# Performance work log

Measured on AMD Instinct MI355X. Metric: run time of the kernel, lower is better.

Reference implementation:

```python
import jax, jax.numpy as jnp
import numpy as np

B, LQ, LK, D = 16, 2048, 2048, 64
TEMPERATURE = 8.0  # sqrt(d_k)


def setup_inputs() -> dict:
    key = jax.random.key(0)
    kq, kk, kv, km = jax.random.split(key, 4)
    q = jax.random.normal(kq, (B, LQ, D), dtype=jnp.float32)
    k = jax.random.normal(kk, (B, LK, D), dtype=jnp.float32)
    v = jax.random.normal(kv, (B, LK, D), dtype=jnp.float32)
    mask = jax.random.randint(km, (B, LQ, LK), 0, 2).astype(jnp.bool_)
    return {"q": q, "k": k, "v": v, "mask": mask}


def reference(q, k, v, mask):
    # attn = bmm(q, k^T) / temperature  -> [B, LQ, LK]
    attn = jnp.einsum("bqd,bkd->bqk", q, k) / TEMPERATURE
    attn = jnp.where(mask, -jnp.inf, attn)
    attn = jax.nn.softmax(attn, axis=2)
    out = jnp.einsum("bqk,bkd->bqd", attn, v)  # [B, LQ, D]
    return out, attn
```

## Files before the change

kernel.cpp:

```cpp
#include <hip/hip_runtime.h>
#include <hip/hip_bf16.h>

namespace {
constexpr int kB = 16;
constexpr int kLQ = 2048;
constexpr int kLK = 2048;
constexpr int kD = 64;
constexpr int kQBlk = 16;
constexpr int kStride = 2056;
constexpr float kLog2e = 1.44269504088896340736f;
}

using short8 = __attribute__((ext_vector_type(8))) short;
using f32x4 = __attribute__((ext_vector_type(4))) float;

union S8U { short8 v; unsigned u[4]; unsigned long long q[2]; };

static __device__ __forceinline__ unsigned pk2(float lo, float hi) {
    __hip_bfloat162 h = __float22bfloat162_rn(float2{lo, hi});
    unsigned short a = __builtin_bit_cast(unsigned short, h.x);
    unsigned short b = __builtin_bit_cast(unsigned short, h.y);
    return (unsigned)a | ((unsigned)b << 16);
}
static __device__ __forceinline__ float bf2f(unsigned short s) {
    unsigned u = ((unsigned)s) << 16;
    return __builtin_bit_cast(float, u);
}
static __device__ __forceinline__ short8 cvt8(float4 a, float4 b) {
    S8U r;
    r.u[0] = pk2(a.x, a.y); r.u[1] = pk2(a.z, a.w);
    r.u[2] = pk2(b.x, b.y); r.u[3] = pk2(b.z, b.w);
    return r.v;
}

__global__ __launch_bounds__(512, 4) void sdpa_v5_kernel(
    const float* __restrict__ qg, const float* __restrict__ kg,
    const float* __restrict__ vg, const void* __restrict__ maskg,
    float* __restrict__ outg, float* __restrict__ attng)
{
    __shared__ unsigned short s_s[kQBlk][kStride];
    __shared__ float s_wsum[8][16];
    __shared__ float s_red[kQBlk][kD];
    __shared__ int s_flag;

    const int tid = threadIdx.x;
    const int wave = tid >> 6;
    const int lane = tid & 63;
    const int r16 = lane & 15;
    const int g = lane >> 4;

    const int blk = blockIdx.x;
    const int b = blk >> 7;
    const int qrow0 = (blk & 127) * kQBlk;

    if (tid < 64) {
        unsigned w = ((const unsigned*)maskg)[tid];
        unsigned long long bal = __ballot((w & 0xFFFFFF00u) != 0u);
        if (tid == 0) s_flag = (bal != 0ull) ? 1 : 0;
    }
    __syncthreads();
    const bool mask_byte = (s_flag != 0);
    const unsigned char* mask_u8 = (const unsigned char*)maskg;
    const int* mask_i32 = (const int*)maskg;

    short8 q0, q1;
    {
        const float4* qp = (const float4*)(qg + ((size_t)b * kLQ + qrow0 + r16) * kD);
        const float s = 0.125f * kLog2e;
        float4 x0 = qp[2*g + 0], x1 = qp[2*g + 1];
        float4 x2 = qp[2*g + 8], x3 = qp[2*g + 9];
        x0 *= s; x1 *= s; x2 *= s; x3 *= s;
        q0 = cvt8(x0, x1);
        q1 = cvt8(x2, x3);
    }
    const size_t kbase = (size_t)b * kLK * kD;
    const size_t mrowL = ((size_t)b * kLQ + qrow0 + r16) * (size_t)kLK;
    float wsum = 0.f;

    unsigned hmA[8], hmB[8];
    if (mask_byte) {
#pragma unroll
        for (int i = 0; i < 8; ++i) {
            const int c0 = (wave + 8 * i) * 32;
            hmA[i] = *(const unsigned*)(mask_u8 + mrowL + c0 + 4*g);
            hmB[i] = *(const unsigned*)(mask_u8 + mrowL + c0 + 16 + 4*g);
        }
    }

    float4 cur[8], nxt[8];
    {
        const int col0 = wave * 32;
        const float4* kpA = (const float4*)(kg + kbase + (size_t)(col0 + r16) * kD);
        const float4* kpB = (const float4*)(kg + kbase + (size_t)(col0 + 16 + r16) * kD);
        cur[0] = kpA[2*g]; cur[1] = kpA[2*g+1]; cur[2] = kpA[2*g+8]; cur[3] = kpA[2*g+9];
        cur[4] = kpB[2*g]; cur[5] = kpB[2*g+1]; cur[6] = kpB[2*g+8]; cur[7] = kpB[2*g+9];
    }
#pragma unroll
    for (int i = 0; i < 8; ++i) {
        const int t = wave + 8 * i;
        const int col0 = t * 32;
        if (i < 7) {
            const int nc0 = (t + 8) * 32;
            const float4* kpA = (const float4*)(kg + kbase + (size_t)(nc0 + r16) * kD);
            const float4* kpB = (const float4*)(kg + kbase + (size_t)(nc0 + 16 + r16) * kD);
            nxt[0] = kpA[2*g]; nxt[1] = kpA[2*g+1]; nxt[2] = kpA[2*g+8]; nxt[3] = kpA[2*g+9];
            nxt[4] = kpB[2*g]; nxt[5] = kpB[2*g+1]; nxt[6] = kpB[2*g+8]; nxt[7] = kpB[2*g+9];
        }
        const short8 kA0 = cvt8(cur[0], cur[1]);
        const short8 kA1 = cvt8(cur[2], cur[3]);
        const short8 kB0 = cvt8(cur[4], cur[5]);
        const short8 kB1 = cvt8(cur[6], cur[7]);
        f32x4 accA = {0.f, 0.f, 0.f, 0.f}, accB = {0.f, 0.f, 0.f, 0.f};
        accA = __builtin_amdgcn_mfma_f32_16x16x32_bf16(kA0, q0, accA, 0, 0, 0);
        accA = __builtin_amdgcn_mfma_f32_16x16x32_bf16(kA1, q1, accA, 0, 0, 0);
        accB = __builtin_amdgcn_mfma_f32_16x16x32_bf16(kB0, q0, accB, 0, 0, 0);
        accB = __builtin_amdgcn_mfma_f32_16x16x32_bf16(kB1, q1, accB, 0, 0, 0);

        const int cA = col0 + 4*g;
        const int cB = col0 + 16 + 4*g;
        unsigned mwA, mwB;
        if (mask_byte) {
            mwA = hmA[i]; mwB = hmB[i];
        } else {
            const int4 a = *(const int4*)(mask_i32 + mrowL + cA);
            const int4 c = *(const int4*)(mask_i32 + mrowL + cB);
            mwA = (a.x ? 1u : 0u) | (a.y ? 0x100u : 0u) | (a.z ? 0x10000u : 0u) | (a.w ? 0x1000000u : 0u);
            mwB = (c.x ? 1u : 0u) | (c.y ? 0x100u : 0u) | (c.z ? 0x10000u : 0u) | (c.w ? 0x1000000u : 0u);
        }
        float eA[4], eB[4];
#pragma unroll
        for (int r = 0; r < 4; ++r) {
            eA[r] = ((mwA >> (8*r)) & 0xFFu) ? 0.f : __builtin_amdgcn_exp2f(accA[r]);
            eB[r] = ((mwB >> (8*r)) & 0xFFu) ? 0.f : __builtin_amdgcn_exp2f(accB[r]);
        }
        wsum += (eA[0] + eA[1]) + (eA[2] + eA[3]) + (eB[0] + eB[1]) + (eB[2] + eB[3]);
        S8U pA, pB;
        pA.u[0] = pk2(eA[0], eA[1]); pA.u[1] = pk2(eA[2], eA[3]);
        pB.u[0] = pk2(eB[0], eB[1]); pB.u[1] = pk2(eB[2], eB[3]);
        *(unsigned long long*)&s_s[r16][cA] = pA.q[0];
        *(unsigned long long*)&s_s[r16][cB] = pB.q[0];
#pragma unroll
        for (int j = 0; j < 8; ++j) cur[j] = nxt[j];
    }
    wsum += __shfl_xor(wsum, 16, 64);
    wsum += __shfl_xor(wsum, 32, 64);
    if (g == 0) s_wsum[wave][r16] = wsum;
    __syncthreads();

    {
        const int rr = tid >> 5;
        const int cc = tid & 31;
        float rsum = 0.f;
#pragma unroll
        for (int w = 0; w < 8; ++w) rsum += s_wsum[w][rr];
        const float rinv = __builtin_amdgcn_rcpf(rsum);
        float* arow = attng + ((size_t)b * kLQ + qrow0 + rr) * kLK;
#pragma unroll 4
        for (int i = 0; i < 16; ++i) {
            const int col = cc * 4 + i * 128;
            const unsigned long long sv = *(const unsigned long long*)&s_s[rr][col];
            float4 a;
            a.x = bf2f((unsigned short)(sv >>  0)) * rinv;
            a.y = bf2f((unsigned short)(sv >> 16)) * rinv;
            a.z = bf2f((unsigned short)(sv >> 32)) * rinv;
            a.w = bf2f((unsigned short)(sv >> 48)) * rinv;
            *(float4*)(arow + col) = a;
        }
    }

    {
        const int d0 = (wave & 3) * 16;
        const int kh = wave >> 2;
        const float* vbase = vg + (size_t)b * kLK * kD + d0 + r16;
        float va[8], vb[8];
#pragma unroll
        for (int j = 0; j < 8; ++j) va[j] = vbase[(size_t)(kh*1024 + 8*g + j) * kD];
        f32x4 acc = {0.f, 0.f, 0.f, 0.f};
#pragma unroll
        for (int kt = 0; kt < 32; ++kt) {
            const int kk0 = (kh * 32 + kt) * 32 + 8 * g;
            float* cv = (kt & 1) ? vb : va;
            float* nv = (kt & 1) ? va : vb;
            if (kt < 31) {
#pragma unroll
                for (int j = 0; j < 8; ++j) nv[j] = vbase[(size_t)(kk0 + 32 + j) * kD];
            }
            const short8 af = *(const short8*)&s_s[r16][kk0];
            S8U bv;
            bv.u[0] = pk2(cv[0], cv[1]); bv.u[1] = pk2(cv[2], cv[3]);
            bv.u[2] = pk2(cv[4], cv[5]); bv.u[3] = pk2(cv[6], cv[7]);
            acc = __builtin_amdgcn_mfma_f32_16x16x32_bf16(af, bv.v, acc, 0, 0, 0);
        }
        if (kh == 1) {
#pragma unroll
            for (int r = 0; r < 4; ++r) s_red[4*g + r][d0 + r16] = acc[r];
        }
        __syncthreads();
        if (kh == 0) {
#pragma unroll
            for (int r = 0; r < 4; ++r) {
                const int m = 4*g + r;
                float rs = 0.f;
#pragma unroll
                for (int w = 0; w < 8; ++w) rs += s_wsum[w][m];
                outg[((size_t)b * kLQ + qrow0 + m) * kD + d0 + r16] =
                    (acc[r] + s_red[m][d0 + r16]) * __builtin_amdgcn_rcpf(rs);
            }
        }
    }
}

extern "C" void kernel_launch(void* const* d_in, const int* in_sizes, int n_in,
                              void* d_out, int out_size, void* d_ws, size_t ws_size,
                              hipStream_t stream) {
    (void)in_sizes; (void)n_in; (void)out_size; (void)d_ws; (void)ws_size;
    const float* q = (const float*)d_in[0];
    const float* k = (const float*)d_in[1];
    const float* v = (const float*)d_in[2];
    const void* mask = d_in[3];
    float* out = (float*)d_out;
    float* attn = out + (size_t)kB * kLQ * kD;
    const dim3 grid(kB * (kLQ / kQBlk));
    sdpa_v5_kernel<<<grid, 512, 0, stream>>>(q, k, v, mask, out, attn);
}
```

Measured before the change: 278.1 us.

## Split fused attention into QK-exp kernel and normalize-PV kernel

Replaces the single fused kernel with two kernels. The first tiles 64 query rows by 512 keys, stages K and mask in shared memory, writes unnormalized exp scores to the attn buffer and partial row sums into the out buffer. The second reads those back, normalizes them in place, and computes P·V. This adds a full extra read and write of the large attn matrix and a second launch, in exchange for K reuse across more query rows and lower shared-memory use per block.

```diff
diff --git a/kernel.cpp b/kernel.cpp
--- a/kernel.cpp
+++ b/kernel.cpp
@@ -6,15 +6,20 @@
 constexpr int kLQ = 2048;
 constexpr int kLK = 2048;
 constexpr int kD = 64;
-constexpr int kQBlk = 16;
-constexpr int kStride = 2056;
 constexpr float kLog2e = 1.44269504088896340736f;
+constexpr int kQT = 64;
+constexpr int kKT = 512;
+constexpr int kKStrB = 144;
+constexpr int kMStrB = 40;
+constexpr int kBStrB = 144;
+constexpr int kChunk = 256;
+constexpr int kEStrB = 528;
 }
 
 using short8 = __attribute__((ext_vector_type(8))) short;
 using f32x4 = __attribute__((ext_vector_type(4))) float;
 
-union S8U { short8 v; unsigned u[4]; unsigned long long q[2]; };
+union S8U { short8 v; unsigned u[4]; };
 
 static __device__ __forceinline__ unsigned pk2(float lo, float hi) {
     __hip_bfloat162 h = __float22bfloat162_rn(float2{lo, hi});
@@ -22,25 +27,15 @@
     unsigned short b = __builtin_bit_cast(unsigned short, h.y);
     return (unsigned)a | ((unsigned)b << 16);
 }
-static __device__ __forceinline__ float bf2f(unsigned short s) {
-    unsigned u = ((unsigned)s) << 16;
-    return __builtin_bit_cast(float, u);
-}
-static __device__ __forceinline__ short8 cvt8(float4 a, float4 b) {
-    S8U r;
-    r.u[0] = pk2(a.x, a.y); r.u[1] = pk2(a.z, a.w);
-    r.u[2] = pk2(b.x, b.y); r.u[3] = pk2(b.z, b.w);
-    return r.v;
-}
-
-__global__ __launch_bounds__(512, 4) void sdpa_v5_kernel(
+
+__global__ __launch_bounds__(256, 4) void k1_qke(
     const float* __restrict__ qg, const float* __restrict__ kg,
-    const float* __restrict__ vg, const void* __restrict__ maskg,
-    float* __restrict__ outg, float* __restrict__ attng)
+    const void* __restrict__ maskg, float* __restrict__ attng,
+    float* __restrict__ outg)
 {
-    __shared__ unsigned short s_s[kQBlk][kStride];
-    __shared__ float s_wsum[8][16];
-    __shared__ float s_red[kQBlk][kD];
+    __shared__ __align__(16) unsigned char s_kst[32 * kKStrB];
+    __shared__ __align__(16) unsigned char s_mst[64 * kMStrB];
+    __shared__ __align__(16) unsigned char s_bnc[4][16 * kBStrB];
     __shared__ int s_flag;
 
     const int tid = threadIdx.x;
@@ -51,7 +46,10 @@
 
     const int blk = blockIdx.x;
     const int b = blk >> 7;
-    const int qrow0 = (blk & 127) * kQBlk;
+    const int kt = (blk >> 5) & 3;
+    const int qt = blk & 31;
+    const int rows0 = qt * kQT;
+    const int c0 = kt * kKT;
 
     if (tid < 64) {
         unsigned w = ((const unsigned*)maskg)[tid];
@@ -65,147 +63,168 @@
 
     short8 q0, q1;
     {
-        const float4* qp = (const float4*)(qg + ((size_t)b * kLQ + qrow0 + r16) * kD);
+        const float4* qp = (const float4*)(qg + ((size_t)b * kLQ + rows0 + wave * 16 + r16) * kD);
         const float s = 0.125f * kLog2e;
         float4 x0 = qp[2*g + 0], x1 = qp[2*g + 1];
         float4 x2 = qp[2*g + 8], x3 = qp[2*g + 9];
         x0 *= s; x1 *= s; x2 *= s; x3 *= s;
-        q0 = cvt8(x0, x1);
-        q1 = cvt8(x2, x3);
-    }
-    const size_t kbase = (size_t)b * kLK * kD;
-    const size_t mrowL = ((size_t)b * kLQ + qrow0 + r16) * (size_t)kLK;
+        S8U a, c;
+        a.u[0] = pk2(x0.x, x0.y); a.u[1] = pk2(x0.z, x0.w);
+        a.u[2] = pk2(x1.x, x1.y); a.u[3] = pk2(x1.z, x1.w);
+        c.u[0] = pk2(x2.x, x2.y); c.u[1] = pk2(x2.z, x2.w);
+        c.u[2] = pk2(x3.x, x3.y); c.u[3] = pk2(x3.z, x3.w);
+        q0 = a.v; q1 = c.v;
+    }
+
     float wsum = 0.f;
 
-    unsigned hmA[8], hmB[8];
-    if (mask_byte) {
-#pragma unroll
-        for (int i = 0; i < 8; ++i) {
-            const int c0 = (wave + 8 * i) * 32;
-            hmA[i] = *(const unsigned*)(mask_u8 + mrowL + c0 + 4*g);
-            hmB[i] = *(const unsigned*)(mask_u8 + mrowL + c0 + 16 + 4*g);
-        }
-    }
-
-    float4 cur[8], nxt[8];
-    {
-        const int col0 = wave * 32;
-        const float4* kpA = (const float4*)(kg + kbase + (size_t)(col0 + r16) * kD);
-        const float4* kpB = (const float4*)(kg + kbase + (size_t)(col0 + 16 + r16) * kD);
-        cur[0] = kpA[2*g]; cur[1] = kpA[2*g+1]; cur[2] = kpA[2*g+8]; cur[3] = kpA[2*g+9];
-        cur[4] = kpB[2*g]; cur[5] = kpB[2*g+1]; cur[6] = kpB[2*g+8]; cur[7] = kpB[2*g+9];
-    }
-#pragma unroll
-    for (int i = 0; i < 8; ++i) {
-        const int t = wave + 8 * i;
-        const int col0 = t * 32;
-        if (i < 7) {
-            const int nc0 = (t + 8) * 32;
-            const float4* kpA = (const float4*)(kg + kbase + (size_t)(nc0 + r16) * kD);
-            const float4* kpB = (const float4*)(kg + kbase + (size_t)(nc0 + 16 + r16) * kD);
-            nxt[0] = kpA[2*g]; nxt[1] = kpA[2*g+1]; nxt[2] = kpA[2*g+8]; nxt[3] = kpA[2*g+9];
-            nxt[4] = kpB[2*g]; nxt[5] = kpB[2*g+1]; nxt[6] = kpB[2*g+8]; nxt[7] = kpB[2*g+9];
-        }
-        const short8 kA0 = cvt8(cur[0], cur[1]);
-        const short8 kA1 = cvt8(cur[2], cur[3]);
-        const short8 kB0 = cvt8(cur[4], cur[5]);
-        const short8 kB1 = cvt8(cur[6], cur[7]);
+    for (int sub = 0; sub < kKT / 32; ++sub) {
+        const int csub = c0 + sub * 32;
+        {
+            const int krow = tid >> 3;
+            const int d8 = (tid & 7) * 8;
+            const float4* kp = (const float4*)(kg + ((size_t)b * kLK + csub + krow) * kD + d8);
+            float4 y0 = kp[0], y1 = kp[1];
+            S8U p;
+            p.u[0] = pk2(y0.x, y0.y); p.u[1] = pk2(y0.z, y0.w);
+            p.u[2] = pk2(y1.x, y1.y); p.u[3] = pk2(y1.z, y1.w);
+            *(short8*)(s_kst + krow * kKStrB + d8 * 2) = p.v;
+        }
+        {
+            const int mrow = tid >> 2;
+            const int mc = (tid & 3) * 8;
+            unsigned long long f;
+            if (mask_byte) {
+                f = *(const unsigned long long*)(mask_u8 +
+                        ((size_t)b * kLQ + rows0 + mrow) * (size_t)kLK + csub + mc);
+            } else {
+                const int* mp = mask_i32 + ((size_t)b * kLQ + rows0 + mrow) * (size_t)kLK + csub + mc;
+                const int4 m0 = *(const int4*)mp;
+                const int4 m1 = *(const int4*)(mp + 4);
+                f  = (m0.x ? 1ull : 0ull)       | (m0.y ? 1ull << 8 : 0ull)
+                   | (m0.z ? 1ull << 16 : 0ull) | (m0.w ? 1ull << 24 : 0ull)
+                   | (m1.x ? 1ull << 32 : 0ull) | (m1.y ? 1ull << 40 : 0ull)
+                   | (m1.z ? 1ull << 48 : 0ull) | (m1.w ? 1ull << 56 : 0ull);
+            }
+            *(unsigned long long*)(s_mst + mrow * kMStrB + mc) = f;
+        }
+        __syncthreads();
+
+        const short8 kA0 = *(const short8*)(s_kst + r16 * kKStrB + g * 16);
+        const short8 kA1 = *(const short8*)(s_kst + r16 * kKStrB + 64 + g * 16);
+        const short8 kB0 = *(const short8*)(s_kst + (16 + r16) * kKStrB + g * 16);
+        const short8 kB1 = *(const short8*)(s_kst + (16 + r16) * kKStrB + 64 + g * 16);
         f32x4 accA = {0.f, 0.f, 0.f, 0.f}, accB = {0.f, 0.f, 0.f, 0.f};
         accA = __builtin_amdgcn_mfma_f32_16x16x32_bf16(kA0, q0, accA, 0, 0, 0);
         accA = __builtin_amdgcn_mfma_f32_16x16x32_bf16(kA1, q1, accA, 0, 0, 0);
         accB = __builtin_amdgcn_mfma_f32_16x16x32_bf16(kB0, q0, accB, 0, 0, 0);
         accB = __builtin_amdgcn_mfma_f32_16x16x32_bf16(kB1, q1, accB, 0, 0, 0);
 
-        const int cA = col0 + 4*g;
-        const int cB = col0 + 16 + 4*g;
-        unsigned mwA, mwB;
-        if (mask_byte) {
-            mwA = hmA[i]; mwB = hmB[i];
-        } else {
-            const int4 a = *(const int4*)(mask_i32 + mrowL + cA);
-            const int4 c = *(const int4*)(mask_i32 + mrowL + cB);
-            mwA = (a.x ? 1u : 0u) | (a.y ? 0x100u : 0u) | (a.z ? 0x10000u : 0u) | (a.w ? 0x1000000u : 0u);
-            mwB = (c.x ? 1u : 0u) | (c.y ? 0x100u : 0u) | (c.z ? 0x10000u : 0u) | (c.w ? 0x1000000u : 0u);
-        }
-        float eA[4], eB[4];
+        const unsigned mwA = *(const unsigned*)(s_mst + (wave * 16 + r16) * kMStrB + 4 * g);
+        const unsigned mwB = *(const unsigned*)(s_mst + (wave * 16 + r16) * kMStrB + 16 + 4 * g);
+        f32x4 eA, eB;
 #pragma unroll
         for (int r = 0; r < 4; ++r) {
             eA[r] = ((mwA >> (8*r)) & 0xFFu) ? 0.f : __builtin_amdgcn_exp2f(accA[r]);
             eB[r] = ((mwB >> (8*r)) & 0xFFu) ? 0.f : __builtin_amdgcn_exp2f(accB[r]);
         }
         wsum += (eA[0] + eA[1]) + (eA[2] + eA[3]) + (eB[0] + eB[1]) + (eB[2] + eB[3]);
-        S8U pA, pB;
-        pA.u[0] = pk2(eA[0], eA[1]); pA.u[1] = pk2(eA[2], eA[3]);
-        pB.u[0] = pk2(eB[0], eB[1]); pB.u[1] = pk2(eB[2], eB[3]);
-        *(unsigned long long*)&s_s[r16][cA] = pA.q[0];
-        *(unsigned long long*)&s_s[r16][cB] = pB.q[0];
-#pragma unroll
-        for (int j = 0; j < 8; ++j) cur[j] = nxt[j];
+        *(f32x4*)(s_bnc[wave] + r16 * kBStrB + g * 16) = eA;
+        *(f32x4*)(s_bnc[wave] + r16 * kBStrB + 64 + g * 16) = eB;
+        __syncthreads();
+
+        {
+            const int row = tid >> 2;
+            const int cseg = tid & 3;
+            const unsigned char* src = s_bnc[row >> 4] + (row & 15) * kBStrB + cseg * 32;
+            const f32x4 v0 = *(const f32x4*)src;
+            const f32x4 v1 = *(const f32x4*)(src + 16);
+            float* dst = attng + ((size_t)b * kLQ + rows0 + row) * (size_t)kLK + csub + cseg * 8;
+            *(f32x4*)dst = v0;
+            *(f32x4*)(dst + 4) = v1;
+        }
     }
     wsum += __shfl_xor(wsum, 16, 64);
     wsum += __shfl_xor(wsum, 32, 64);
-    if (g == 0) s_wsum[wave][r16] = wsum;
+    if (g == 0)
+        outg[((size_t)b * kLQ + rows0 + wave * 16 + r16) * kD + kt] = wsum;
+}
+
+__global__ __launch_bounds__(512, 2) void k2_norm_pv(
+    const float* __restrict__ vg, float* __restrict__ attng,
+    float* __restrict__ outg)
+{
+    __shared__ __align__(16) unsigned char s_e[16 * kEStrB];
+    __shared__ float s_red[16][kD];
+    __shared__ float s_rinv[16];
+
+    const int tid = threadIdx.x;
+    const int wave = tid >> 6;
+    const int lane = tid & 63;
+    const int r16 = lane & 15;
+    const int g = lane >> 4;
+
+    const int blk = blockIdx.x;
+    const int b = blk >> 7;
+    const int row0 = (blk & 127) * 16;
+
+    if (tid < 64) {
+        const int r = tid >> 2, p = tid & 3;
+        float ps = outg[((size_t)b * kLQ + row0 + r) * kD + p];
+        ps += __shfl_xor(ps, 1, 64);
+        ps += __shfl_xor(ps, 2, 64);
+        if (p == 0) s_rinv[r] = __builtin_amdgcn_rcpf(ps);
+    }
     __syncthreads();
 
-    {
-        const int rr = tid >> 5;
-        const int cc = tid & 31;
-        float rsum = 0.f;
-#pragma unroll
-        for (int w = 0; w < 8; ++w) rsum += s_wsum[w][rr];
-        const float rinv = __builtin_amdgcn_rcpf(rsum);
-        float* arow = attng + ((size_t)b * kLQ + qrow0 + rr) * kLK;
-#pragma unroll 4
-        for (int i = 0; i < 16; ++i) {
-            const int col = cc * 4 + i * 128;
-            const unsigned long long sv = *(const unsigned long long*)&s_s[rr][col];
-            float4 a;
-            a.x = bf2f((unsigned short)(sv >>  0)) * rinv;
-            a.y = bf2f((unsigned short)(sv >> 16)) * rinv;
-            a.z = bf2f((unsigned short)(sv >> 32)) * rinv;
-            a.w = bf2f((unsigned short)(sv >> 48)) * rinv;
-            *(float4*)(arow + col) = a;
-        }
-    }
-
-    {
-        const int d0 = (wave & 3) * 16;
-        const int kh = wave >> 2;
-        const float* vbase = vg + (size_t)b * kLK * kD + d0 + r16;
-        float va[8], vb[8];
-#pragma unroll
-        for (int j = 0; j < 8; ++j) va[j] = vbase[(size_t)(kh*1024 + 8*g + j) * kD];
-        f32x4 acc = {0.f, 0.f, 0.f, 0.f};
-#pragma unroll
-        for (int kt = 0; kt < 32; ++kt) {
-            const int kk0 = (kh * 32 + kt) * 32 + 8 * g;
-            float* cv = (kt & 1) ? vb : va;
-            float* nv = (kt & 1) ? va : vb;
-            if (kt < 31) {
-#pragma unroll
-                for (int j = 0; j < 8; ++j) nv[j] = vbase[(size_t)(kk0 + 32 + j) * kD];
-            }
-            const short8 af = *(const short8*)&s_s[r16][kk0];
+    const int d0 = (wave & 3) * 16;
+    const int kh = wave >> 2;
+    f32x4 acc = {0.f, 0.f, 0.f, 0.f};
+    const float* vbase = vg + (size_t)b * kLK * kD + d0 + r16;
+
+    for (int chunk = 0; chunk < kLK / kChunk; ++chunk) {
+        const int c0 = chunk * kChunk;
+        {
+            const int row = tid >> 5;
+            const int cc = tid & 31;
+            const float rinv = s_rinv[row];
+            float* ap = attng + ((size_t)b * kLQ + row0 + row) * (size_t)kLK + c0 + cc * 8;
+            f32x4 e0 = *(const f32x4*)ap;
+            f32x4 e1 = *(const f32x4*)(ap + 4);
+            e0 *= rinv; e1 *= rinv;
+            *(f32x4*)ap = e0;
+            *(f32x4*)(ap + 4) = e1;
+            S8U p;
+            p.u[0] = pk2(e0[0], e0[1]); p.u[1] = pk2(e0[2], e0[3]);
+            p.u[2] = pk2(e1[0], e1[1]); p.u[3] = pk2(e1[2], e1[3]);
+            *(short8*)(s_e + row * kEStrB + cc * 16) = p.v;
+        }
+        __syncthreads();
+#pragma unroll
+        for (int s = 0; s < 4; ++s) {
+            const int kk = kh * 128 + s * 32 + 8 * g;
+            const short8 af = *(const short8*)(s_e + r16 * kEStrB + kk * 2);
+            const float* vp = vbase + (size_t)(c0 + kk) * kD;
+            float v0 = vp[0*kD], v1 = vp[1*kD], v2 = vp[2*kD], v3 = vp[3*kD];
+            float v4 = vp[4*kD], v5 = vp[5*kD], v6 = vp[6*kD], v7 = vp[7*kD];
             S8U bv;
-            bv.u[0] = pk2(cv[0], cv[1]); bv.u[1] = pk2(cv[2], cv[3]);
-            bv.u[2] = pk2(cv[4], cv[5]); bv.u[3] = pk2(cv[6], cv[7]);
+            bv.u[0] = pk2(v0, v1); bv.u[1] = pk2(v2, v3);
+            bv.u[2] = pk2(v4, v5); bv.u[3] = pk2(v6, v7);
             acc = __builtin_amdgcn_mfma_f32_16x16x32_bf16(af, bv.v, acc, 0, 0, 0);
         }
-        if (kh == 1) {
-#pragma unroll
-            for (int r = 0; r < 4; ++r) s_red[4*g + r][d0 + r16] = acc[r];
-        }
-        __syncthreads();
-        if (kh == 0) {
-#pragma unroll
-            for (int r = 0; r < 4; ++r) {
-                const int m = 4*g + r;
-                float rs = 0.f;
-#pragma unroll
-                for (int w = 0; w < 8; ++w) rs += s_wsum[w][m];
-                outg[((size_t)b * kLQ + qrow0 + m) * kD + d0 + r16] =
-                    (acc[r] + s_red[m][d0 + r16]) * __builtin_amdgcn_rcpf(rs);
-            }
+        __syncthreads();
+    }
+
+    if (kh == 1) {
+#pragma unroll
+        for (int r = 0; r < 4; ++r) s_red[4*g + r][d0 + r16] = acc[r];
+    }
+    __syncthreads();
+    if (kh == 0) {
+#pragma unroll
+        for (int r = 0; r < 4; ++r) {
+            const int m = 4*g + r;
+            outg[((size_t)b * kLQ + row0 + m) * kD + d0 + r16] = acc[r] + s_red[m][d0 + r16];
         }
     }
 }
@@ -220,6 +239,6 @@
     const void* mask = d_in[3];
     float* out = (float*)d_out;
     float* attn = out + (size_t)kB * kLQ * kD;
-    const dim3 grid(kB * (kLQ / kQBlk));
-    sdpa_v5_kernel<<<grid, 512, 0, stream>>>(q, k, v, mask, out, attn);
-}
+    k1_qke<<<dim3(kB * 128), 256, 0, stream>>>(q, k, mask, attn, out);
+    k2_norm_pv<<<dim3(kB * 128), 512, 0, stream>>>(v, attn, out);
+}
```

Result: slower. 285.4 us (+2.6%).
